# Kernel optimization log

Hardware: AMD Instinct MI355X
Metric: run time of the kernel (lower is better)

## Reference

```python
import jax, jax.numpy as jnp
import numpy as np

H = 512  # hidden_dim
F = 512  # feat_vec_dim
N_LEAVES = 2048
BATCH = 8


def _tree_indices(n_leaves, batch_size):
    """Complete-binary-tree forest, nodes numbered bottom-up per tree:
    leaves 0..L-1, then L..L+L/2-1, ..., root last. Returns per-non-leaf-layer
    son/fa global index arrays (concatenated over the batch of trees)."""
    npt = 2 * n_leaves - 1  # nodes per tree
    levels = []
    start, size = 0, n_leaves
    while size >= 1:
        levels.append((start, size))
        start += size
        size //= 2
    offs = np.arange(batch_size) * npt
    def idx(l):
        s, sz = levels[l]
        return jnp.asarray((offs[:, None] + np.arange(s, s + sz)[None, :]).reshape(-1))
    n_layers = len(levels) - 1  # number of non-leaf layers (11 here)
    son = [idx(l) for l in range(n_layers)]
    fa = [idx(l + 1) for l in range(n_layers)]
    return son, fa, npt * batch_size, n_layers


def setup_inputs() -> dict:
    key = jax.random.key(0)
    ks = jax.random.split(key, 24)
    n_total = (2 * N_LEAVES - 1) * BATCH  # 32760
    s = 1.0 / np.sqrt(F)
    mk = lambda k: jax.random.normal(k, (H, F), dtype=jnp.float32) * s
    vk = lambda k: jax.random.normal(k, (H,), dtype=jnp.float32) * 0.02
    return {
        "feat_vec": jax.random.normal(ks[0], (n_total, F), dtype=jnp.float32),
        "Wh": mk(ks[1]), "Wz": mk(ks[2]), "Wr": mk(ks[3]),
        "Uh": mk(ks[4]), "Uz": mk(ks[5]), "bUz": vk(ks[6]),
        "Ur": mk(ks[7]), "bUr": vk(ks[8]),
        "Whd": mk(ks[9]), "Wzd": mk(ks[10]), "Wrd": mk(ks[11]),
        "Uhd": mk(ks[12]), "Uzd": mk(ks[13]), "bUzd": vk(ks[14]),
        "Urd": mk(ks[15]), "bUrd": vk(ks[16]),
        "W1": mk(ks[17]), "b1": jax.random.normal(ks[18], (F,), dtype=jnp.float32) * 0.02,
        "W2": mk(ks[19]), "b2": jax.random.normal(ks[20], (F,), dtype=jnp.float32) * 0.02,
        "n_leaves": N_LEAVES,
        "batch_size": BATCH,
    }


def reference(feat_vec, Wh, Wz, Wr, Uh, Uz, bUz, Ur, bUr,
              Whd, Wzd, Wrd, Uhd, Uzd, bUzd, Urd, bUrd,
              W1, b1, W2, b2, n_leaves, batch_size):
    son, fa, n_total, n_layers = _tree_indices(int(n_leaves), int(batch_size))
    sig, tanh = jax.nn.sigmoid, jnp.tanh

    # ---- bottom-up tree GRU ----
    h = jnp.zeros((n_total, H), dtype=feat_vec.dtype)
    # leaves: h = (1-z) * tanh(Wh x), z = sigmoid(Wz x)
    x0 = feat_vec[son[0]]
    z0 = sig(x0 @ Wz.T)
    h = h.at[son[0]].set((1.0 - z0) * tanh(x0 @ Wh.T))
    for l in range(n_layers):
        # A_T_sub @ h_son == sum of each father's two contiguous children
        h_son = h[son[l]]
        h_sum = h_son.reshape(-1, 2, H).sum(axis=1)
        x = feat_vec[fa[l]]
        z = sig(x @ Wz.T + h_sum @ Uz.T + bUz)
        r = sig(x @ Wr.T + h_sum @ Ur.T + bUr)
        cand = tanh(x @ Wh.T + (r * h_sum) @ Uh.T)
        h = h.at[fa[l]].set(z * h_sum + (1.0 - z) * cand)

    # ---- top-down tree GRU ----
    hd = jnp.zeros((n_total, H), dtype=feat_vec.dtype)
    roots = fa[n_layers - 1]
    hd = hd.at[roots].set(h[roots])
    for l in range(n_layers - 1, -1, -1):
        # A_sub @ hd_fa == each son gathers its (single) father's state
        h_fa = jnp.repeat(hd[fa[l]], 2, axis=0)
        x = feat_vec[son[l]]
        zd = sig(x @ Wzd.T + h_fa @ Uzd.T + bUzd)
        rd = sig(x @ Wrd.T + h_fa @ Urd.T + bUrd)
        cand = tanh(x @ Whd.T + (rd * h_fa) @ Uhd.T)
        hd = hd.at[son[l]].set(zd * h_fa + (1.0 - zd) * cand)

    # out = FFN1(h) + FFN2(hd)
    return h @ W1.T + b1 + hd @ W2.T + b2
```

## Files before the change

### kernel.cpp

```cpp
#include <hip/hip_runtime.h>
#include <hip/hip_bf16.h>
#include <cmath>
#include <cstdint>

#define NPT 4095
#define NT  32760
#define FD  512

using bf16 = __hip_bfloat16;
using bf8v = __attribute__((ext_vector_type(8))) short;
using us8v = __attribute__((ext_vector_type(8))) unsigned short;
using f4v  = __attribute__((ext_vector_type(4))) float;

__device__ __forceinline__ float b2f(bf16 x){ return __bfloat162float(x); }
__device__ __forceinline__ bf16  f2b(float x){ return __float2bfloat16(x); }
__device__ __forceinline__ float us2f(unsigned short u){ union{unsigned int i; float f;} v; v.i = ((unsigned)u)<<16; return v.f; }
__device__ __forceinline__ unsigned short f2us(float f){ union{bf16 b; unsigned short u;} v; v.b = __float2bfloat16(f); return v.u; }

__device__ __forceinline__ float fast_sig(float x){
  float e = __builtin_amdgcn_exp2f(-1.4426950408889634f * x);
  return __builtin_amdgcn_rcpf(1.f + e);
}
__device__ __forceinline__ float fast_tanh(float x){
  float ax = fabsf(x);
  float e = __builtin_amdgcn_exp2f(-2.885390081777927f * ax);
  float r = (1.f - e) * __builtin_amdgcn_rcpf(1.f + e);
  return copysignf(r, x);
}

__device__ __forceinline__ void gload_lds16(const bf16* g, bf16* l){
  __builtin_amdgcn_global_load_lds(
    (const __attribute__((address_space(1))) unsigned int*)g,
    (__attribute__((address_space(3))) unsigned int*)l, 16, 0, 0);
}


__global__ void cvt_b16(bf16* __restrict__ dst, const float* __restrict__ src, int n8){
  int e = blockIdx.x*256 + threadIdx.x;
  if (e >= n8) return;
  const float4* s = (const float4*)(src + (size_t)e*8);
  float4 a = s[0], b = s[1];
  us8v o = { f2us(a.x), f2us(a.y), f2us(a.z), f2us(a.w),
             f2us(b.x), f2us(b.y), f2us(b.z), f2us(b.w) };
  *(us8v*)(dst + (size_t)e*8) = o;
}

struct PackArgs { const float* s[16]; bf16* d[16]; int dk[16]; int ro[16]; int co[16]; };
__global__ void pack_all(PackArgs pa){
  int idx = blockIdx.x >> 7;
  int e = (blockIdx.x & 127)*256 + threadIdx.x;
  int r = e >> 6, c8 = e & 63;
  const float4* s = (const float4*)(pa.s[idx] + (size_t)r*512 + c8*8);
  float4 a = s[0], b = s[1];
  us8v o = { f2us(a.x), f2us(a.y), f2us(a.z), f2us(a.w),
             f2us(b.x), f2us(b.y), f2us(b.z), f2us(b.w) };
  *(us8v*)(pa.d[idx] + (size_t)(pa.ro[idx] + r)*pa.dk[idx] + pa.co[idx] + c8*8) = o;
}

__global__ void leaf_combine(bf16* __restrict__ h_b, bf16* __restrict__ s0,
                             const bf16* __restrict__ xwzr, const bf16* __restrict__ tb){
  int e = blockIdx.x*256 + threadIdx.x;
  int j = e >> 6, c8 = e & 63;
  int m0 = 2*j;
  int tree = m0 >> 11, pos = m0 & 2047;
  size_t node = (size_t)tree*NPT + pos;
  us8v z0 = *(const us8v*)(xwzr + node*1024 + c8*8);
  us8v z1 = *(const us8v*)(xwzr + (node+1)*1024 + c8*8);
  size_t i0 = (size_t)m0*FD + c8*8;
  us8v t0 = *(const us8v*)(tb + i0);
  us8v t1 = *(const us8v*)(tb + i0 + FD);
  us8v h0, h1, sv;
  #pragma unroll
  for (int i = 0; i < 8; ++i){
    float a = (1.f - fast_sig(us2f(z0[i]))) * us2f(t0[i]);
    float b = (1.f - fast_sig(us2f(z1[i]))) * us2f(t1[i]);
    h0[i] = f2us(a); h1[i] = f2us(b); sv[i] = f2us(a + b);
  }
  *(us8v*)(h_b + node*FD + c8*8) = h0;
  *(us8v*)(h_b + (node+1)*FD + c8*8) = h1;
  *(us8v*)(s0 + (size_t)j*FD + c8*8) = sv;
}

__global__ void roots_k(bf16* __restrict__ hd, bf16* __restrict__ sA, const bf16* __restrict__ h){
  int e = blockIdx.x*256 + threadIdx.x;
  int t = e >> 6, c8 = e & 63;
  size_t off = ((size_t)t*NPT + 4094)*FD + c8*8;
  us8v v = *(const us8v*)(h + off);
  *(us8v*)(hd + off) = v;
  *(us8v*)(sA + (size_t)(2*t)*FD + c8*8) = v;
  *(us8v*)(sA + (size_t)(2*t+1)*FD + c8*8) = v;
}

__device__ __forceinline__ void epi4(
    const f4v& a, int rbase, int n, int M, int mode,
    const float* __restrict__ bias0, const float* __restrict__ bias1,
    const bf16* __restrict__ zb, const bf16* __restrict__ sb,
    const bf16* __restrict__ xw,
    bf16* __restrict__ o0, bf16* __restrict__ o1,
    bf16* __restrict__ hO, float* __restrict__ outF,
    int o_start, int o_log2, bf16* __restrict__ sN, int smode)
{
  if (rbase >= M) return;
  const int omask = (1 << o_log2) - 1;
  if (mode == 0){
    #pragma unroll
    for (int i = 0; i < 4; ++i){
      int row = rbase + i; if (row >= M) break;
      o1[(size_t)row*FD + n] = f2b(fast_tanh(a[i]));
    }
  } else if (mode == 3){
    #pragma unroll
    for (int i = 0; i < 4; ++i){
      int row = rbase + i; if (row >= M) break;
      o0[(size_t)row*1024 + n] = f2b(a[i]);
    }
  } else if (mode == 1){
    #pragma unroll
    for (int i = 0; i < 4; ++i){
      int row = rbase + i; if (row >= M) break;
      int tree = row >> o_log2, pos = row & omask;
      float v = a[i] + b2f(xw[((size_t)tree*NPT + o_start + pos)*1024 + n]);
      if (n < 512){
        o0[(size_t)row*FD + n] = f2b(fast_sig(v + bias0[n]));
      } else {
        float r = fast_sig(v + bias1[n-512]);
        size_t off = (size_t)row*FD + (n-512);
        o1[off] = f2b(r * b2f(sb[off]));
      }
    }
  } else if (mode == 4){
    #pragma unroll
    for (int i = 0; i < 4; ++i){
      int row = rbase + i; if (row >= M) break;
      outF[(size_t)row*FD + n] = a[i] + bias0[n] + bias1[n];
    }
  } else {
    float hv[4];
    #pragma unroll
    for (int i = 0; i < 4; ++i){
      int row = rbase + i;
      if (row >= M){ hv[i] = 0.f; continue; }
      float c = fast_tanh(a[i]);
      size_t off = (size_t)row*FD + n;
      float z = b2f(zb[off]);
      float s = b2f(sb[off]);
      float h = z*s + (1.f - z)*c;
      hv[i] = h;
      int tree = row >> o_log2, pos = row & omask;
      hO[((size_t)tree*NPT + o_start + pos)*FD + n] = f2b(h);
    }
    if (smode == 1){
      if (rbase + 1 < M) sN[(size_t)(rbase>>1)*FD + n] = f2b(hv[0] + hv[1]);
      if (rbase + 3 < M) sN[(size_t)((rbase>>1) + 1)*FD + n] = f2b(hv[2] + hv[3]);
    } else if (smode == 2){
      #pragma unroll
      for (int i = 0; i < 4; ++i){
        int row = rbase + i; if (row >= M) break;
        bf16 hb = f2b(hv[i]);
        sN[(size_t)(2*row)*FD + n] = hb;
        sN[(size_t)(2*row+1)*FD + n] = hb;
      }
    }
  }
}

__global__ __launch_bounds__(256) void gemm_big(
    const bf16* __restrict__ A0, const bf16* __restrict__ A1,
    const bf16* __restrict__ Wp, int M, int K, int ldb,
    int a_start, int a_log2, int o_start, int o_log2,
    const float* __restrict__ bias0, const float* __restrict__ bias1,
    const bf16* __restrict__ zb, const bf16* __restrict__ sb,
    const bf16* __restrict__ xw,
    bf16* __restrict__ o0, bf16* __restrict__ o1,
    bf16* __restrict__ hO, float* __restrict__ outF,
    bf16* __restrict__ sN, int smode, int mode)
{
  __shared__ bf16 As[128*64];
  __shared__ bf16 Bs[128*64];

  const int t = threadIdx.x, lane = t & 63, wid = t >> 6;
  const int wr = wid >> 1, wc = wid & 1;
  const int lr = lane & 15, quad = lane >> 4;
  const int m_blk = blockIdx.x*128, n_blk = blockIdx.y*128;
  const int Mm1 = M - 1;
  const int amask = (1 << a_log2) - 1;
  const int wbase = (t & ~63);

  const bf16* a0p[4]; const bf16* a1p[4]; const bf16* bp[4];
  #pragma unroll
  for (int p = 0; p < 4; ++p){
    int c = p*256 + t;
    int rl = c >> 3, slot = c & 7;
    int g = slot ^ (rl & 7);
    int r = m_blk + rl; if (r > Mm1) r = Mm1;
    int tr = r >> a_log2, po = r & amask;
    a0p[p] = A0 + ((size_t)tr*NPT + a_start + po)*FD + g*8;
    a1p[p] = A1 + (size_t)r*FD + g*8;
    bp[p]  = Wp + (size_t)(n_blk + rl)*ldb + g*8;
  }

  f4v acc[4][4] = {};

  for (int k0 = 0; k0 < K; k0 += 64){
    #pragma unroll
    for (int p = 0; p < 4; ++p){
      const bf16* src = (k0 < 512) ? (a0p[p] + k0) : (a1p[p] + (k0 - 512));
      gload_lds16(src, &As[(size_t)(p*256 + wbase)*8]);
    }
    #pragma unroll
    for (int p = 0; p < 4; ++p)
      gload_lds16(bp[p] + k0, &Bs[(size_t)(p*256 + wbase)*8]);
    __syncthreads();

    #pragma unroll
    for (int kh = 0; kh < 2; ++kh){
      int cidx = kh*4 + quad;
      bf8v af[4], bv[4];
      #pragma unroll
      for (int i = 0; i < 4; ++i){
        int ra = wr*64 + i*16 + lr;
        af[i] = *(const bf8v*)&As[ra*64 + ((cidx ^ (ra & 7))*8)];
        int rb = wc*64 + i*16 + lr;
        bv[i] = *(const bf8v*)&Bs[rb*64 + ((cidx ^ (rb & 7))*8)];
      }
      #pragma unroll
      for (int i = 0; i < 4; ++i)
        #pragma unroll
        for (int j = 0; j < 4; ++j)
          acc[i][j] = __builtin_amdgcn_mfma_f32_16x16x32_bf16(af[i], bv[j], acc[i][j], 0, 0, 0);
    }
    __syncthreads();
  }

  #pragma unroll
  for (int mt = 0; mt < 4; ++mt){
    int rbase = m_blk + wr*64 + mt*16 + quad*4;
    #pragma unroll
    for (int nt = 0; nt < 4; ++nt){
      int n = n_blk + wc*64 + nt*16 + lr;
      epi4(acc[mt][nt], rbase, n, M, mode, bias0, bias1, zb, sb, xw, o0, o1, hO, outF,
           o_start, o_log2, sN, smode);
    }
  }
}

__global__ __launch_bounds__(256) void gemm_small(
    const bf16* __restrict__ A0, const bf16* __restrict__ A1,
    const bf16* __restrict__ Wp, int M, int K, int ldb,
    int a_start, int a_log2, int o_start, int o_log2,
    const float* __restrict__ bias0, const float* __restrict__ bias1,
    const bf16* __restrict__ zb, const bf16* __restrict__ sb,
    const bf16* __restrict__ xw,
    bf16* __restrict__ o0, bf16* __restrict__ o1,
    bf16* __restrict__ hO, float* __restrict__ outF,
    bf16* __restrict__ sN, int smode, int mode)
{
  const int lane = threadIdx.x & 63, wid = threadIdx.x >> 6;
  const int wr = wid >> 1, wc = wid & 1;
  const int m_base = blockIdx.x*64 + wr*32;
  const int n_base = blockIdx.y*64 + wc*32;
  const int lr = lane & 15, quad = lane >> 4;
  const int Mm1 = M - 1;
  const int amask = (1 << a_log2) - 1;

  f4v acc[2][2] = {};

  const bf16 *a0p[2], *a1p[2], *bp[2];
  #pragma unroll
  for (int mt = 0; mt < 2; ++mt){
    int m = m_base + mt*16 + lr; if (m > Mm1) m = Mm1;
    int tr = m >> a_log2, po = m & amask;
    a0p[mt] = A0 + ((size_t)tr*NPT + a_start + po)*FD;
    a1p[mt] = A1 + (size_t)m*FD;
  }
  #pragma unroll
  for (int nt = 0; nt < 2; ++nt)
    bp[nt] = Wp + (size_t)(n_base + nt*16 + lr)*ldb;

  for (int k0 = 0; k0 < K; k0 += 32){
    int k = k0 + quad*8;
    bf8v a[2], b[2];
    #pragma unroll
    for (int mt = 0; mt < 2; ++mt)
      a[mt] = *(const bf8v*)((k0 < 512) ? (a0p[mt] + k) : (a1p[mt] + (k - 512)));
    #pragma unroll
    for (int nt = 0; nt < 2; ++nt)
      b[nt] = *(const bf8v*)(bp[nt] + k);
    #pragma unroll
    for (int mt = 0; mt < 2; ++mt)
      #pragma unroll
      for (int nt = 0; nt < 2; ++nt)
        acc[mt][nt] = __builtin_amdgcn_mfma_f32_16x16x32_bf16(a[mt], b[nt], acc[mt][nt], 0, 0, 0);
  }

  #pragma unroll
  for (int mt = 0; mt < 2; ++mt){
    int rbase = m_base + mt*16 + quad*4;
    #pragma unroll
    for (int nt = 0; nt < 2; ++nt){
      int n = n_base + nt*16 + lr;
      epi4(acc[mt][nt], rbase, n, M, mode, bias0, bias1, zb, sb, xw, o0, o1, hO, outF,
           o_start, o_log2, sN, smode);
    }
  }
}


extern "C" void kernel_launch(void* const* d_in, const int* in_sizes, int n_in,
                              void* d_out, int out_size, void* d_ws, size_t ws_size,
                              hipStream_t stream)
{
  const float* feat = (const float*)d_in[0];
  const float* Wh   = (const float*)d_in[1];
  const float* Wz   = (const float*)d_in[2];
  const float* Wr   = (const float*)d_in[3];
  const float* Uh   = (const float*)d_in[4];
  const float* Uz   = (const float*)d_in[5];
  const float* bUz  = (const float*)d_in[6];
  const float* Ur   = (const float*)d_in[7];
  const float* bUr  = (const float*)d_in[8];
  const float* Whd  = (const float*)d_in[9];
  const float* Wzd  = (const float*)d_in[10];
  const float* Wrd  = (const float*)d_in[11];
  const float* Uhd  = (const float*)d_in[12];
  const float* Uzd  = (const float*)d_in[13];
  const float* bUzd = (const float*)d_in[14];
  const float* Urd  = (const float*)d_in[15];
  const float* bUrd = (const float*)d_in[16];
  const float* W1   = (const float*)d_in[17];
  const float* b1   = (const float*)d_in[18];
  const float* W2   = (const float*)d_in[19];
  const float* b2   = (const float*)d_in[20];
  float* out = (float*)d_out;

  int starts[12], szs[12];
  { int s = 0, sz = 2048; for (int l = 0; l < 12; ++l){ starts[l] = s; szs[l] = sz; s += sz; sz >>= 1; } }

  char* p = (char*)d_ws;
  auto take = [&](size_t b)->char*{ char* q = p; p += (b + 255) & ~(size_t)255; return q; };
  bf16* featb = (bf16*)take((size_t)NT*FD*2);
  bf16* h_b   = (bf16*)take((size_t)NT*FD*2);
  bf16* hd_b  = (bf16*)take((size_t)NT*FD*2);
  bf16* Wzr_u = (bf16*)take((size_t)1024*512*2);
  bf16* Wzr_d = (bf16*)take((size_t)1024*512*2);
  bf16* Uzr_u = (bf16*)take((size_t)1024*512*2);
  bf16* Uzr_d = (bf16*)take((size_t)1024*512*2);
  bf16* Whu   = (bf16*)take((size_t)512*1024*2);
  bf16* Whu_d = (bf16*)take((size_t)512*1024*2);
  bf16* Wout  = (bf16*)take((size_t)512*1024*2);
  bf16* z16   = (bf16*)take((size_t)16384*512*2);
  bf16* t16   = (bf16*)take((size_t)16384*512*2);
  bf16* rh16  = (bf16*)take((size_t)16384*512*2);
  bf16* sP0   = (bf16*)take((size_t)16384*512*2);
  bf16* sP1   = (bf16*)take((size_t)16384*512*2);
  if ((size_t)(p - (char*)d_ws) > ws_size) return;

  bf16* xWzr = (bf16*)d_out;

  cvt_b16<<<(NT*FD/8 + 255)/256, 256, 0, stream>>>(featb, feat, NT*FD/8);
  PackArgs pa;
  int pi = 0;
  auto pk = [&](const float* src, bf16* dst, int dk, int ro, int co){
    pa.s[pi] = src; pa.d[pi] = dst; pa.dk[pi] = dk; pa.ro[pi] = ro; pa.co[pi] = co; ++pi;
  };
  pk(Wz, Wzr_u, 512, 0, 0);    pk(Wr, Wzr_u, 512, 512, 0);
  pk(Wzd, Wzr_d, 512, 0, 0);   pk(Wrd, Wzr_d, 512, 512, 0);
  pk(Uz, Uzr_u, 512, 0, 0);    pk(Ur, Uzr_u, 512, 512, 0);
  pk(Uzd, Uzr_d, 512, 0, 0);   pk(Urd, Uzr_d, 512, 512, 0);
  pk(Wh, Whu, 1024, 0, 0);     pk(Uh, Whu, 1024, 0, 512);
  pk(Whd, Whu_d, 1024, 0, 0);  pk(Uhd, Whu_d, 1024, 0, 512);
  pk(W1, Wout, 1024, 0, 0);    pk(W2, Wout, 1024, 0, 512);
  pack_all<<<14*128, 256, 0, stream>>>(pa);

  auto gemm = [&](const bf16* A0, const bf16* A1, const bf16* Wp, int M, int N, int K, int ldb,
                  int a_start, int a_log2, int o_start, int o_log2,
                  const float* bias0, const float* bias1,
                  const bf16* zb, const bf16* sb, const bf16* xw,
                  bf16* o0, bf16* o1, bf16* hO, float* outF,
                  bf16* sN, int smode, int mode){
    if (M >= 2048){
      dim3 g((M + 127)/128, N/128);
      gemm_big<<<g, 256, 0, stream>>>(A0, A1, Wp, M, K, ldb, a_start, a_log2, o_start, o_log2,
                                      bias0, bias1, zb, sb, xw, o0, o1, hO, outF, sN, smode, mode);
    } else {
      dim3 g((M + 63)/64, N/64);
      gemm_small<<<g, 256, 0, stream>>>(A0, A1, Wp, M, K, ldb, a_start, a_log2, o_start, o_log2,
                                        bias0, bias1, zb, sb, xw, o0, o1, hO, outF, sN, smode, mode);
    }
  };

  gemm(featb, featb, Wzr_u, NT, 1024, 512, 512, 0, 26, 0, 26,
       nullptr, nullptr, nullptr, nullptr, nullptr, xWzr, nullptr, nullptr, nullptr, nullptr, 0, 3);

  gemm(featb, featb, Whu, 16384, 512, 512, 1024, 0, 11, 0, 11,
       nullptr, nullptr, nullptr, nullptr, nullptr, nullptr, t16, nullptr, nullptr, nullptr, 0, 0);
  leaf_combine<<<2048, 256, 0, stream>>>(h_b, sP0, xWzr, t16);

  for (int l = 0; l < 11; ++l){
    int Mf = 8*szs[l+1];
    int al2 = 10 - l, os = starts[l+1];
    bf16* sCur = (l & 1) ? sP1 : sP0;
    bf16* sNext = (l & 1) ? sP0 : sP1;
    int smode = (l < 10) ? 1 : 0;
    gemm(sCur, sCur, Uzr_u, Mf, 1024, 512, 512, 0, 26, os, al2,
         bUz, bUr, nullptr, sCur, xWzr, z16, rh16, nullptr, nullptr, nullptr, 0, 1);
    gemm(featb, rh16, Whu, Mf, 512, 1024, 1024, os, al2, os, al2,
         nullptr, nullptr, z16, sCur, nullptr, nullptr, nullptr, h_b, nullptr, sNext, smode, 2);
  }

  gemm(featb, featb, Wzr_d, NT, 1024, 512, 512, 0, 26, 0, 26,
       nullptr, nullptr, nullptr, nullptr, nullptr, xWzr, nullptr, nullptr, nullptr, nullptr, 0, 3);

  roots_k<<<2, 256, 0, stream>>>(hd_b, sP0, h_b);

  for (int l = 10; l >= 0; --l){
    int Ms = 8*szs[l];
    int al2 = 11 - l, os = starts[l];
    bf16* sCur = ((10 - l) & 1) ? sP1 : sP0;
    bf16* sNext = ((10 - l) & 1) ? sP0 : sP1;
    int smode = (l > 0) ? 2 : 0;
    gemm(sCur, sCur, Uzr_d, Ms, 1024, 512, 512, 0, 26, os, al2,
         bUzd, bUrd, nullptr, sCur, xWzr, z16, rh16, nullptr, nullptr, nullptr, 0, 1);
    gemm(featb, rh16, Whu_d, Ms, 512, 1024, 1024, os, al2, os, al2,
         nullptr, nullptr, z16, sCur, nullptr, nullptr, nullptr, hd_b, nullptr, sNext, smode, 2);
  }

  gemm(h_b, hd_b, Wout, NT, 512, 1024, 1024, 0, 26, 0, 26,
       b1, b2, nullptr, nullptr, nullptr, nullptr, nullptr, nullptr, out, nullptr, 0, 4);
}
```

Before: 1.419 ms.

## Stage GEMM epilogue through LDS, fuse leaf combine, remap workgroups per XCD

The large GEMM kernel now writes its accumulators to shared memory and re-reads them so each thread handles 8 contiguous columns, giving 16-byte vectorized global loads and stores in every epilogue mode. A new mode 5 fuses the leaf GRU combine (sigmoid gate, tanh, pair-sum) into the leaf GEMM, so the t16 intermediate buffer and the separate leaf_combine kernel are no longer needed. Workgroup IDs are also remapped so consecutive tiles land on the same XCD, which is meant to improve L2 locality. The cost is a 64KB LDS tile, which may lower occupancy, plus an extra block-wide barrier.

```diff
diff --git a/kernel.cpp b/kernel.cpp
--- a/kernel.cpp
+++ b/kernel.cpp
@@ -55,30 +55,6 @@
   us8v o = { f2us(a.x), f2us(a.y), f2us(a.z), f2us(a.w),
              f2us(b.x), f2us(b.y), f2us(b.z), f2us(b.w) };
   *(us8v*)(pa.d[idx] + (size_t)(pa.ro[idx] + r)*pa.dk[idx] + pa.co[idx] + c8*8) = o;
-}
-
-__global__ void leaf_combine(bf16* __restrict__ h_b, bf16* __restrict__ s0,
-                             const bf16* __restrict__ xwzr, const bf16* __restrict__ tb){
-  int e = blockIdx.x*256 + threadIdx.x;
-  int j = e >> 6, c8 = e & 63;
-  int m0 = 2*j;
-  int tree = m0 >> 11, pos = m0 & 2047;
-  size_t node = (size_t)tree*NPT + pos;
-  us8v z0 = *(const us8v*)(xwzr + node*1024 + c8*8);
-  us8v z1 = *(const us8v*)(xwzr + (node+1)*1024 + c8*8);
-  size_t i0 = (size_t)m0*FD + c8*8;
-  us8v t0 = *(const us8v*)(tb + i0);
-  us8v t1 = *(const us8v*)(tb + i0 + FD);
-  us8v h0, h1, sv;
-  #pragma unroll
-  for (int i = 0; i < 8; ++i){
-    float a = (1.f - fast_sig(us2f(z0[i]))) * us2f(t0[i]);
-    float b = (1.f - fast_sig(us2f(z1[i]))) * us2f(t1[i]);
-    h0[i] = f2us(a); h1[i] = f2us(b); sv[i] = f2us(a + b);
-  }
-  *(us8v*)(h_b + node*FD + c8*8) = h0;
-  *(us8v*)(h_b + (node+1)*FD + c8*8) = h1;
-  *(us8v*)(s0 + (size_t)j*FD + c8*8) = sv;
 }
 
 __global__ void roots_k(bf16* __restrict__ hd, bf16* __restrict__ sA, const bf16* __restrict__ h){
@@ -102,19 +78,7 @@
 {
   if (rbase >= M) return;
   const int omask = (1 << o_log2) - 1;
-  if (mode == 0){
-    #pragma unroll
-    for (int i = 0; i < 4; ++i){
-      int row = rbase + i; if (row >= M) break;
-      o1[(size_t)row*FD + n] = f2b(fast_tanh(a[i]));
-    }
-  } else if (mode == 3){
-    #pragma unroll
-    for (int i = 0; i < 4; ++i){
-      int row = rbase + i; if (row >= M) break;
-      o0[(size_t)row*1024 + n] = f2b(a[i]);
-    }
-  } else if (mode == 1){
+  if (mode == 1){
     #pragma unroll
     for (int i = 0; i < 4; ++i){
       int row = rbase + i; if (row >= M) break;
@@ -127,12 +91,6 @@
         size_t off = (size_t)row*FD + (n-512);
         o1[off] = f2b(r * b2f(sb[off]));
       }
-    }
-  } else if (mode == 4){
-    #pragma unroll
-    for (int i = 0; i < 4; ++i){
-      int row = rbase + i; if (row >= M) break;
-      outF[(size_t)row*FD + n] = a[i] + bias0[n] + bias1[n];
     }
   } else {
     float hv[4];
@@ -175,13 +133,23 @@
     bf16* __restrict__ hO, float* __restrict__ outF,
     bf16* __restrict__ sN, int smode, int mode)
 {
-  __shared__ bf16 As[128*64];
-  __shared__ bf16 Bs[128*64];
+  __shared__ __align__(16) char smemraw[128*128*4];
+  bf16* As = (bf16*)smemraw;
+  bf16* Bs = As + 128*64;
+  float* Cf = (float*)smemraw;
 
   const int t = threadIdx.x, lane = t & 63, wid = t >> 6;
   const int wr = wid >> 1, wc = wid & 1;
   const int lr = lane & 15, quad = lane >> 4;
-  const int m_blk = blockIdx.x*128, n_blk = blockIdx.y*128;
+
+  const int gx = gridDim.x;
+  int nwg = gx * gridDim.y;
+  int id = blockIdx.y * gx + blockIdx.x;
+  int q = nwg >> 3, r8 = nwg & 7;
+  int xcd = id & 7, jj = id >> 3;
+  int wg = (xcd < r8 ? xcd*(q+1) : r8*(q+1) + (xcd - r8)*q) + jj;
+  const int m_blk = (wg % gx) * 128, n_blk = (wg / gx) * 128;
+
   const int Mm1 = M - 1;
   const int amask = (1 << a_log2) - 1;
   const int wbase = (t & ~63);
@@ -234,14 +202,156 @@
 
   #pragma unroll
   for (int mt = 0; mt < 4; ++mt){
-    int rbase = m_blk + wr*64 + mt*16 + quad*4;
+    int r = wr*64 + mt*16 + quad*4;
     #pragma unroll
     for (int nt = 0; nt < 4; ++nt){
-      int n = n_blk + wc*64 + nt*16 + lr;
-      epi4(acc[mt][nt], rbase, n, M, mode, bias0, bias1, zb, sb, xw, o0, o1, hO, outF,
-           o_start, o_log2, sN, smode);
-    }
-  }
+      int c = wc*64 + nt*16 + lr;
+      #pragma unroll
+      for (int i = 0; i < 4; ++i)
+        Cf[(r+i)*128 + c] = acc[mt][nt][i];
+    }
+  }
+  __syncthreads();
+
+  const int r0l = (t >> 4) * 8;
+  const int c0l = (t & 15) * 8;
+  const int gr = m_blk + r0l;
+  const int n0 = n_blk + c0l;
+  if (gr >= M) return;
+  const int omask = (1 << o_log2) - 1;
+
+  #define LOADV(i, vv) { float4 _v0 = *(const float4*)&Cf[(r0l+(i))*128 + c0l]; \
+                         float4 _v1 = *(const float4*)&Cf[(r0l+(i))*128 + c0l + 4]; \
+                         vv[0]=_v0.x; vv[1]=_v0.y; vv[2]=_v0.z; vv[3]=_v0.w; \
+                         vv[4]=_v1.x; vv[5]=_v1.y; vv[6]=_v1.z; vv[7]=_v1.w; }
+
+  if (mode == 3){
+    #pragma unroll
+    for (int i = 0; i < 8; ++i){
+      int row = gr + i; if (row >= M) continue;
+      float vv[8]; LOADV(i, vv);
+      us8v o;
+      #pragma unroll
+      for (int k2 = 0; k2 < 8; ++k2) o[k2] = f2us(vv[k2]);
+      *(us8v*)(o0 + (size_t)row*1024 + n0) = o;
+    }
+  } else if (mode == 4){
+    float bb[8];
+    *(float4*)&bb[0] = *(const float4*)&bias0[n0];
+    *(float4*)&bb[4] = *(const float4*)&bias0[n0+4];
+    float b2v[8];
+    *(float4*)&b2v[0] = *(const float4*)&bias1[n0];
+    *(float4*)&b2v[4] = *(const float4*)&bias1[n0+4];
+    #pragma unroll
+    for (int k2 = 0; k2 < 8; ++k2) bb[k2] += b2v[k2];
+    #pragma unroll
+    for (int i = 0; i < 8; ++i){
+      int row = gr + i; if (row >= M) continue;
+      float vv[8]; LOADV(i, vv);
+      float4 o0v = { vv[0]+bb[0], vv[1]+bb[1], vv[2]+bb[2], vv[3]+bb[3] };
+      float4 o1v = { vv[4]+bb[4], vv[5]+bb[5], vv[6]+bb[6], vv[7]+bb[7] };
+      *(float4*)(outF + (size_t)row*FD + n0)     = o0v;
+      *(float4*)(outF + (size_t)row*FD + n0 + 4) = o1v;
+    }
+  } else if (mode == 1){
+    if (n0 < 512){
+      float bb[8];
+      *(float4*)&bb[0] = *(const float4*)&bias0[n0];
+      *(float4*)&bb[4] = *(const float4*)&bias0[n0+4];
+      #pragma unroll
+      for (int i = 0; i < 8; ++i){
+        int row = gr + i; if (row >= M) continue;
+        size_t node = (size_t)(row >> o_log2)*NPT + o_start + (row & omask);
+        us8v xv = *(const us8v*)(xw + node*1024 + n0);
+        float vv[8]; LOADV(i, vv);
+        us8v o;
+        #pragma unroll
+        for (int k2 = 0; k2 < 8; ++k2)
+          o[k2] = f2us(fast_sig(vv[k2] + us2f(xv[k2]) + bb[k2]));
+        *(us8v*)(o0 + (size_t)row*FD + n0) = o;
+      }
+    } else {
+      int n5 = n0 - 512;
+      float bb[8];
+      *(float4*)&bb[0] = *(const float4*)&bias1[n5];
+      *(float4*)&bb[4] = *(const float4*)&bias1[n5+4];
+      #pragma unroll
+      for (int i = 0; i < 8; ++i){
+        int row = gr + i; if (row >= M) continue;
+        size_t node = (size_t)(row >> o_log2)*NPT + o_start + (row & omask);
+        us8v xv = *(const us8v*)(xw + node*1024 + n0);
+        us8v sv = *(const us8v*)(sb + (size_t)row*FD + n5);
+        float vv[8]; LOADV(i, vv);
+        us8v o;
+        #pragma unroll
+        for (int k2 = 0; k2 < 8; ++k2){
+          float r = fast_sig(vv[k2] + us2f(xv[k2]) + bb[k2]);
+          o[k2] = f2us(r * us2f(sv[k2]));
+        }
+        *(us8v*)(o1 + (size_t)row*FD + n5) = o;
+      }
+    }
+  } else if (mode == 5){
+    float hprev[8];
+    #pragma unroll
+    for (int i = 0; i < 8; ++i){
+      int row = gr + i; if (row >= M) continue;
+      size_t node = (size_t)(row >> o_log2)*NPT + o_start + (row & omask);
+      us8v zv = *(const us8v*)(xw + node*1024 + n0);
+      float vv[8]; LOADV(i, vv);
+      float hc[8]; us8v hb;
+      #pragma unroll
+      for (int k2 = 0; k2 < 8; ++k2){
+        float h = (1.f - fast_sig(us2f(zv[k2]))) * fast_tanh(vv[k2]);
+        hc[k2] = h; hb[k2] = f2us(h);
+      }
+      *(us8v*)(hO + node*FD + n0) = hb;
+      if (i & 1){
+        us8v ss;
+        #pragma unroll
+        for (int k2 = 0; k2 < 8; ++k2) ss[k2] = f2us(hprev[k2] + hc[k2]);
+        *(us8v*)(sN + (size_t)(row>>1)*FD + n0) = ss;
+      } else {
+        #pragma unroll
+        for (int k2 = 0; k2 < 8; ++k2) hprev[k2] = hc[k2];
+      }
+    }
+  } else {
+    float hprev[8];
+    #pragma unroll
+    for (int i = 0; i < 8; ++i){
+      int row = gr + i; if (row >= M) continue;
+      us8v zv = *(const us8v*)(zb + (size_t)row*FD + n0);
+      us8v sv = *(const us8v*)(sb + (size_t)row*FD + n0);
+      float vv[8]; LOADV(i, vv);
+      float hc[8]; us8v hb;
+      #pragma unroll
+      for (int k2 = 0; k2 < 8; ++k2){
+        float c = fast_tanh(vv[k2]);
+        float z = us2f(zv[k2]);
+        float s = us2f(sv[k2]);
+        float h = z*s + (1.f - z)*c;
+        hc[k2] = h; hb[k2] = f2us(h);
+      }
+      size_t node = (size_t)(row >> o_log2)*NPT + o_start + (row & omask);
+      *(us8v*)(hO + node*FD + n0) = hb;
+      if (smode == 1){
+        if (i & 1){
+          us8v ss;
+          #pragma unroll
+          for (int k2 = 0; k2 < 8; ++k2) ss[k2] = f2us(hprev[k2] + hc[k2]);
+          *(us8v*)(sN + (size_t)(row>>1)*FD + n0) = ss;
+        } else {
+          #pragma unroll
+          for (int k2 = 0; k2 < 8; ++k2) hprev[k2] = hc[k2];
+        }
+      } else if (smode == 2){
+        *(us8v*)(sN + (size_t)(2*row)*FD + n0) = hb;
+        *(us8v*)(sN + (size_t)(2*row+1)*FD + n0) = hb;
+      }
+    }
+  }
+  #undef LOADV
 }
 
 __global__ __launch_bounds__(256) void gemm_small(
@@ -349,7 +459,6 @@
   bf16* Whu_d = (bf16*)take((size_t)512*1024*2);
   bf16* Wout  = (bf16*)take((size_t)512*1024*2);
   bf16* z16   = (bf16*)take((size_t)16384*512*2);
-  bf16* t16   = (bf16*)take((size_t)16384*512*2);
   bf16* rh16  = (bf16*)take((size_t)16384*512*2);
   bf16* sP0   = (bf16*)take((size_t)16384*512*2);
   bf16* sP1   = (bf16*)take((size_t)16384*512*2);
@@ -393,8 +502,7 @@
        nullptr, nullptr, nullptr, nullptr, nullptr, xWzr, nullptr, nullptr, nullptr, nullptr, 0, 3);
 
   gemm(featb, featb, Whu, 16384, 512, 512, 1024, 0, 11, 0, 11,
-       nullptr, nullptr, nullptr, nullptr, nullptr, nullptr, t16, nullptr, nullptr, nullptr, 0, 0);
-  leaf_combine<<<2048, 256, 0, stream>>>(h_b, sP0, xWzr, t16);
+       nullptr, nullptr, nullptr, nullptr, xWzr, nullptr, nullptr, h_b, nullptr, sP0, 1, 5);
 
   for (int l = 0; l < 11; ++l){
     int Mf = 8*szs[l+1];
```

New measurement: 1.204 ms. -15.1%, faster.
